# Optimization experiments

Hardware: AMD Instinct MI355X
Metric: run time of the kernel (lower is better)

The kernel has to match this reference:

```python
import jax, jax.numpy as jnp
import numpy as np

N = 50000   # nodes
E = 800000  # directed edges
IN, H1, H2, OUT = 128, 64, 32, 40
K = 2       # SGConv hops


def setup_inputs() -> dict:
    key = jax.random.key(0)
    ks = jax.random.split(key, 8)
    x = jax.random.normal(ks[0], (N, IN), dtype=jnp.float32)
    edge_index = jax.random.randint(ks[1], (2, E), 0, N, dtype=jnp.int64)
    s = lambda k, shp, fan: jax.random.normal(k, shp, dtype=jnp.float32) / np.sqrt(fan)
    return {
        "x": x,
        "edge_index": edge_index,
        "W1": s(ks[2], (IN, H1), IN), "b1": jnp.zeros((H1,), jnp.float32),
        "W2": s(ks[3], (H1, H2), H1), "b2": jnp.zeros((H2,), jnp.float32),
        "Wf": s(ks[4], (H2, OUT), H2), "bf": jnp.zeros((OUT,), jnp.float32),
    }


def _gcn_norm(edge_index, num_nodes):
    # add self-loops, then norm = d^{-1/2}[src] * d^{-1/2}[dst], d over targets
    loop = jnp.arange(num_nodes, dtype=edge_index.dtype)
    src = jnp.concatenate([edge_index[0], loop])
    dst = jnp.concatenate([edge_index[1], loop])
    deg = jax.ops.segment_sum(jnp.ones_like(src, dtype=jnp.float32), dst,
                              num_segments=num_nodes)
    dinv = jnp.where(deg > 0, jax.lax.rsqrt(deg), 0.0)
    norm = dinv[src] * dinv[dst]  # [E + N]
    return src, dst, norm


def _propagate_k(x, src, dst, norm, num_nodes, k):
    for _ in range(k):
        x = jax.ops.segment_sum(x[src] * norm[:, None], dst,
                                num_segments=num_nodes)
    return x


def reference(x, edge_index, W1, b1, W2, b2, Wf, bf):
    num_nodes = x.shape[0]
    src, dst, norm = _gcn_norm(edge_index, num_nodes)
    # SGConv layer 1: A_hat^K x, then linear, then relu
    h = _propagate_k(x, src, dst, norm, num_nodes, K)
    h = jax.nn.relu(h @ W1 + b1)
    # SGConv layer 2
    h = _propagate_k(h, src, dst, norm, num_nodes, K)
    h = jax.nn.relu(h @ W2 + b2)
    embedding = h
    logits = h @ Wf + bf
    return (embedding, logits)
```

## Files before the change

### kernel.cpp

```cpp
#include <hip/hip_runtime.h>

#define NN 50000
#define NE 800000
#define IN_F 128
#define H1_F 64
#define H2_F 32
#define OUT_F 40

#define BSH 7
#define NBKT 391
#define CAPA 4032
#define CHUNK 4096
#define NCH ((NE + CHUNK - 1) / CHUNK)

static inline int cdiv(int a, int b) { return (a + b - 1) / b; }

__global__ void initcur_k(int* __restrict__ gCursor) {
    int b = blockIdx.x * 256 + threadIdx.x;
    if (b < NBKT) gCursor[b] = b * CAPA;
}

__global__ __launch_bounds__(256)
void binA_k(const int* __restrict__ src, const int* __restrict__ dst,
            uint2* __restrict__ pairs, int* __restrict__ gCursor) {
    __shared__ int hist[512], incl[512], runSt[512], lcur[512], baseSh[512];
    __shared__ uint2 stage[CHUNK];
    const int t = threadIdx.x;
    const int e0 = blockIdx.x * CHUNK;
    const int n = min(CHUNK, NE - e0);

    hist[t] = 0; hist[t + 256] = 0;
    __syncthreads();
    for (int i = t; i < n; i += 256) {
        int d = dst[e0 + i];
        atomicAdd(&hist[d >> BSH], 1);
    }
    __syncthreads();
    incl[t] = hist[t]; incl[t + 256] = hist[t + 256];
    __syncthreads();
    for (int off = 1; off < 512; off <<= 1) {
        int v0 = (t >= off) ? incl[t - off] : 0;
        int v1 = (t + 256 >= off) ? incl[t + 256 - off] : 0;
        __syncthreads();
        incl[t] += v0; incl[t + 256] += v1;
        __syncthreads();
    }
    runSt[t] = incl[t] - hist[t];   runSt[t + 256] = incl[t + 256] - hist[t + 256];
    lcur[t]  = runSt[t];            lcur[t + 256]  = runSt[t + 256];
    __syncthreads();
    for (int i = t; i < n; i += 256) {
        int s = src[e0 + i], d = dst[e0 + i];
        int b = d >> BSH;
        int p = atomicAdd(&lcur[b], 1);
        stage[p] = make_uint2((unsigned)s, (unsigned)d);
    }
    for (int b = t; b < NBKT; b += 256) {
        int c = hist[b];
        baseSh[b] = c ? atomicAdd(&gCursor[b], c) : 0;
    }
    __syncthreads();
    for (int i = t; i < n; i += 256) {
        uint2 p = stage[i];
        int b = (int)(p.y >> BSH);
        int gp = baseSh[b] + (i - runSt[b]);
        if (gp < (b + 1) * CAPA) pairs[gp] = p;
    }
}

__global__ __launch_bounds__(512)
void segscan_k(const int* __restrict__ gCursor, int* __restrict__ segBase) {
    __shared__ int sh[512], orig[512];
    int t = threadIdx.x;
    int c = 0;
    if (t < NBKT) {
        c = gCursor[t] - t * CAPA;
        c = max(0, min(c, CAPA));
    }
    sh[t] = c; orig[t] = c;
    __syncthreads();
    for (int off = 1; off < 512; off <<= 1) {
        int v = (t >= off) ? sh[t - off] : 0;
        __syncthreads();
        sh[t] += v;
        __syncthreads();
    }
    if (t < NBKT) segBase[t] = sh[t] - orig[t];
}

__global__ __launch_bounds__(256)
void binB_k(const uint2* __restrict__ pairs, const int* __restrict__ gCursor,
            const int* __restrict__ segBase, int* __restrict__ cursor,
            float* __restrict__ dinv, int* __restrict__ csr) {
    const int b = blockIdx.x;
    const int nodeBase = b << BSH;
    const int nNodes = min(128, NN - nodeBase);
    int count = gCursor[b] - b * CAPA;
    count = max(0, min(count, CAPA));
    const int seg = segBase[b];
    __shared__ int hist[128], incl[128], lcur[128];
    const int t = threadIdx.x;
    if (t < 128) hist[t] = 0;
    __syncthreads();
    const uint2* bp = pairs + (size_t)b * CAPA;
    for (int i = t; i < count; i += 256) {
        int d = (int)bp[i].y - nodeBase;
        atomicAdd(&hist[d], 1);
    }
    __syncthreads();
    if (t < 128) incl[t] = hist[t];
    __syncthreads();
    for (int off = 1; off < 128; off <<= 1) {
        int v = (t < 128 && t >= off) ? incl[t - off] : 0;
        __syncthreads();
        if (t < 128) incl[t] += v;
        __syncthreads();
    }
    if (t < nNodes) {
        cursor[nodeBase + t] = seg + incl[t];
        dinv[nodeBase + t]   = rsqrtf((float)hist[t] + 1.0f);
        lcur[t] = seg + incl[t] - hist[t];
    }
    __syncthreads();
    for (int i = t; i < count; i += 256) {
        uint2 p = bp[i];
        int d = (int)p.y - nodeBase;
        int pos = atomicAdd(&lcur[d], 1);
        csr[pos] = (int)p.x;
    }
}

template<int K, int F, int CT, int RPT, int BLOCK, bool BIAS, bool SCALE>
__global__ __launch_bounds__(BLOCK)
void gemm_tile_k(const float* __restrict__ X, const float* __restrict__ W,
                 const float* __restrict__ b, const float* __restrict__ dinv,
                 float* __restrict__ Y) {
    constexpr int RT = BLOCK / CT;
    constexpr int TR = RT * RPT;
    constexpr int KT = 32;
    constexpr int KPAD = KT + 1;
    __shared__ float Xs[TR][KPAD];
    __shared__ float Wsh[KT][F];
    const int rowBase = blockIdx.x * TR;
    const int tc = threadIdx.x % CT;
    const int tr = threadIdx.x / CT;

    float acc[RPT][4];
    #pragma unroll
    for (int i = 0; i < RPT; ++i)
        #pragma unroll
        for (int j = 0; j < 4; ++j) acc[i][j] = 0.0f;

    for (int k0 = 0; k0 < K; k0 += KT) {
        constexpr int XL4 = TR * KT / 4;
        for (int l = threadIdx.x; l < XL4; l += BLOCK) {
            int r  = l / (KT / 4);
            int kk = (l % (KT / 4)) * 4;
            float4 v = make_float4(0.f, 0.f, 0.f, 0.f);
            int gr = rowBase + r;
            if (gr < NN) v = *reinterpret_cast<const float4*>(X + (size_t)gr * K + k0 + kk);
            Xs[r][kk + 0] = v.x; Xs[r][kk + 1] = v.y;
            Xs[r][kk + 2] = v.z; Xs[r][kk + 3] = v.w;
        }
        constexpr int WL4 = KT * F / 4;
        for (int l = threadIdx.x; l < WL4; l += BLOCK) {
            int kk = l / (F / 4);
            int c  = (l % (F / 4)) * 4;
            *reinterpret_cast<float4*>(&Wsh[kk][c]) =
                *reinterpret_cast<const float4*>(W + (size_t)(k0 + kk) * F + c);
        }
        __syncthreads();
        #pragma unroll
        for (int kk = 0; kk < KT; ++kk) {
            float wv[4];
            *reinterpret_cast<float4*>(wv) = *reinterpret_cast<const float4*>(&Wsh[kk][tc * 4]);
            #pragma unroll
            for (int i = 0; i < RPT; ++i) {
                float a = Xs[tr * RPT + i][kk];
                acc[i][0] = fmaf(a, wv[0], acc[i][0]);
                acc[i][1] = fmaf(a, wv[1], acc[i][1]);
                acc[i][2] = fmaf(a, wv[2], acc[i][2]);
                acc[i][3] = fmaf(a, wv[3], acc[i][3]);
            }
        }
        __syncthreads();
    }
    #pragma unroll
    for (int i = 0; i < RPT; ++i) {
        int gr = rowBase + tr * RPT + i;
        if (gr < NN) {
            float sc = SCALE ? dinv[gr] : 1.0f;
            float4 v;
            v.x = acc[i][0]; v.y = acc[i][1]; v.z = acc[i][2]; v.w = acc[i][3];
            if (BIAS) {
                v.x += b[tc * 4 + 0]; v.y += b[tc * 4 + 1];
                v.z += b[tc * 4 + 2]; v.w += b[tc * 4 + 3];
            }
            v.x *= sc; v.y *= sc; v.z *= sc; v.w *= sc;
            *reinterpret_cast<float4*>(Y + (size_t)gr * F + tc * 4) = v;
        }
    }
}

template<int F, bool SQ, bool EPI>
__global__ __launch_bounds__(256)
void pull4_k(const float* __restrict__ in, const int* __restrict__ csr,
             const int* __restrict__ cursor, const float* __restrict__ dinv,
             const float* __restrict__ b, float* __restrict__ out) {
    constexpr int LPN = F / 4;
    constexpr int NPB = 256 / LPN;
    const int t = threadIdx.x;
    const int node = blockIdx.x * NPB + t / LPN;
    const int col  = (t % LPN) * 4;
    if (node >= NN) return;
    const int beg = (node == 0) ? 0 : cursor[node - 1];
    const int end = cursor[node];
    const float* base = in + (size_t)node * F + col;
    float4 a0 = *reinterpret_cast<const float4*>(base);
    float4 a1 = make_float4(0.f, 0.f, 0.f, 0.f);
    int k = beg;
    for (; k + 1 < end; k += 2) {
        int s0 = csr[k], s1 = csr[k + 1];
        float4 v0 = *reinterpret_cast<const float4*>(in + (size_t)s0 * F + col);
        float4 v1 = *reinterpret_cast<const float4*>(in + (size_t)s1 * F + col);
        a0.x += v0.x; a0.y += v0.y; a0.z += v0.z; a0.w += v0.w;
        a1.x += v1.x; a1.y += v1.y; a1.z += v1.z; a1.w += v1.w;
    }
    if (k < end) {
        int s0 = csr[k];
        float4 v0 = *reinterpret_cast<const float4*>(in + (size_t)s0 * F + col);
        a0.x += v0.x; a0.y += v0.y; a0.z += v0.z; a0.w += v0.w;
    }
    float sc = dinv[node];
    if (SQ) sc *= sc;
    float4 r;
    r.x = (a0.x + a1.x) * sc; r.y = (a0.y + a1.y) * sc;
    r.z = (a0.z + a1.z) * sc; r.w = (a0.w + a1.w) * sc;
    if (EPI) {
        const float4 bv = *reinterpret_cast<const float4*>(b + col);
        r.x = fmaxf(r.x + bv.x, 0.f); r.y = fmaxf(r.y + bv.y, 0.f);
        r.z = fmaxf(r.z + bv.z, 0.f); r.w = fmaxf(r.w + bv.w, 0.f);
    }
    *reinterpret_cast<float4*>(out + (size_t)node * F + col) = r;
}

extern "C" void kernel_launch(void* const* d_in, const int* in_sizes, int n_in,
                              void* d_out, int out_size, void* d_ws, size_t ws_size,
                              hipStream_t stream) {
    const float* x  = (const float*)d_in[0];
    const int*   ei = (const int*)d_in[1];
    const float* W1 = (const float*)d_in[2];
    const float* b1 = (const float*)d_in[3];
    const float* W2 = (const float*)d_in[4];
    const float* b2 = (const float*)d_in[5];
    const float* Wf = (const float*)d_in[6];
    const float* bf = (const float*)d_in[7];

    float* out    = (float*)d_out;
    float* embOut = out;
    float* logits = out + (size_t)NN * H2_F;

    const int* src = ei;
    const int* dst = ei + NE;

    float* ws       = (float*)d_ws;
    float* dinv     = ws;
    int*   cursor   = (int*)(ws + NN);
    int*   csr      = cursor + NN;
    int*   gCursor  = csr + NE;
    int*   segBase  = gCursor + 512;
    float* bufA     = (float*)(segBase + 512);
    float* bufB     = bufA + (size_t)NN * 64;
    uint2* pairs    = (uint2*)bufB;

    initcur_k<<<cdiv(NBKT, 256), 256, 0, stream>>>(gCursor);
    binA_k<<<NCH, 256, 0, stream>>>(src, dst, pairs, gCursor);
    segscan_k<<<1, 512, 0, stream>>>(gCursor, segBase);
    binB_k<<<NBKT, 256, 0, stream>>>(pairs, gCursor, segBase, cursor, dinv, csr);

    gemm_tile_k<IN_F, H1_F, 16, 4, 256, false, true>
        <<<cdiv(NN, 64), 256, 0, stream>>>(x, W1, nullptr, dinv, bufA);
    pull4_k<H1_F, true, false>
        <<<cdiv(NN, 256 / (H1_F / 4)), 256, 0, stream>>>(bufA, csr, cursor, dinv, nullptr, bufB);
    pull4_k<H1_F, false, true>
        <<<cdiv(NN, 256 / (H1_F / 4)), 256, 0, stream>>>(bufB, csr, cursor, dinv, b1, bufA);

    gemm_tile_k<H1_F, H2_F, 8, 2, 256, false, true>
        <<<cdiv(NN, 64), 256, 0, stream>>>(bufA, W2, nullptr, dinv, bufB);
    pull4_k<H2_F, true, false>
        <<<cdiv(NN, 256 / (H2_F / 4)), 256, 0, stream>>>(bufB, csr, cursor, dinv, nullptr, bufA);
    pull4_k<H2_F, false, true>
        <<<cdiv(NN, 256 / (H2_F / 4)), 256, 0, stream>>>(bufA, csr, cursor, dinv, b2, embOut);

    gemm_tile_k<H2_F, OUT_F, 10, 2, 320, true, false>
        <<<cdiv(NN, 64), 320, 0, stream>>>(embOut, Wf, bf, nullptr, logits);
}
```

Before: 245.1 us.

## Fuse second-hop aggregation with the following dense GEMM and widen gather unroll

The second propagation hop of each layer now runs in one kernel together with the next linear layer. Each block aggregates 64 nodes into shared memory and multiplies them by W2 (or Wf) held in shared memory. This removes two standalone GEMM launches and the global round trip of the intermediate activations. The neighbour gather loop also moves from two to four independent accumulators to expose more memory-level parallelism. The cost is more registers and shared memory per block, and all 256 threads of a block wait at a barrier before the GEMM phase.

```diff
diff --git a/kernel.cpp b/kernel.cpp
--- a/kernel.cpp
+++ b/kernel.cpp
@@ -201,11 +201,11 @@
     }
 }
 
-template<int F, bool SQ, bool EPI>
+template<int F>
 __global__ __launch_bounds__(256)
 void pull4_k(const float* __restrict__ in, const int* __restrict__ csr,
              const int* __restrict__ cursor, const float* __restrict__ dinv,
-             const float* __restrict__ b, float* __restrict__ out) {
+             float* __restrict__ out) {
     constexpr int LPN = F / 4;
     constexpr int NPB = 256 / LPN;
     const int t = threadIdx.x;
@@ -214,33 +214,197 @@
     if (node >= NN) return;
     const int beg = (node == 0) ? 0 : cursor[node - 1];
     const int end = cursor[node];
-    const float* base = in + (size_t)node * F + col;
-    float4 a0 = *reinterpret_cast<const float4*>(base);
+    float4 a0 = *reinterpret_cast<const float4*>(in + (size_t)node * F + col);
     float4 a1 = make_float4(0.f, 0.f, 0.f, 0.f);
+    float4 a2 = make_float4(0.f, 0.f, 0.f, 0.f);
+    float4 a3 = make_float4(0.f, 0.f, 0.f, 0.f);
     int k = beg;
-    for (; k + 1 < end; k += 2) {
-        int s0 = csr[k], s1 = csr[k + 1];
+    for (; k + 3 < end; k += 4) {
+        int s0 = csr[k], s1 = csr[k + 1], s2 = csr[k + 2], s3 = csr[k + 3];
         float4 v0 = *reinterpret_cast<const float4*>(in + (size_t)s0 * F + col);
         float4 v1 = *reinterpret_cast<const float4*>(in + (size_t)s1 * F + col);
+        float4 v2 = *reinterpret_cast<const float4*>(in + (size_t)s2 * F + col);
+        float4 v3 = *reinterpret_cast<const float4*>(in + (size_t)s3 * F + col);
         a0.x += v0.x; a0.y += v0.y; a0.z += v0.z; a0.w += v0.w;
         a1.x += v1.x; a1.y += v1.y; a1.z += v1.z; a1.w += v1.w;
-    }
-    if (k < end) {
+        a2.x += v2.x; a2.y += v2.y; a2.z += v2.z; a2.w += v2.w;
+        a3.x += v3.x; a3.y += v3.y; a3.z += v3.z; a3.w += v3.w;
+    }
+    for (; k < end; ++k) {
         int s0 = csr[k];
         float4 v0 = *reinterpret_cast<const float4*>(in + (size_t)s0 * F + col);
         a0.x += v0.x; a0.y += v0.y; a0.z += v0.z; a0.w += v0.w;
     }
-    float sc = dinv[node];
-    if (SQ) sc *= sc;
+    float sc = dinv[node]; sc *= sc;
     float4 r;
-    r.x = (a0.x + a1.x) * sc; r.y = (a0.y + a1.y) * sc;
-    r.z = (a0.z + a1.z) * sc; r.w = (a0.w + a1.w) * sc;
-    if (EPI) {
-        const float4 bv = *reinterpret_cast<const float4*>(b + col);
-        r.x = fmaxf(r.x + bv.x, 0.f); r.y = fmaxf(r.y + bv.y, 0.f);
-        r.z = fmaxf(r.z + bv.z, 0.f); r.w = fmaxf(r.w + bv.w, 0.f);
-    }
+    r.x = (a0.x + a1.x + a2.x + a3.x) * sc;
+    r.y = (a0.y + a1.y + a2.y + a3.y) * sc;
+    r.z = (a0.z + a1.z + a2.z + a3.z) * sc;
+    r.w = (a0.w + a1.w + a2.w + a3.w) * sc;
     *reinterpret_cast<float4*>(out + (size_t)node * F + col) = r;
+}
+
+__global__ __launch_bounds__(256)
+void pullgemm2_k(const float* __restrict__ in, const int* __restrict__ csr,
+                 const int* __restrict__ cursor, const float* __restrict__ dinv,
+                 const float* __restrict__ b1, const float* __restrict__ W2,
+                 float* __restrict__ outT) {
+    __shared__ float hs[64][68];
+    __shared__ float W2s[64][32];
+    const int t = threadIdx.x;
+    for (int i = t; i < 64 * 32 / 4; i += 256)
+        reinterpret_cast<float4*>(&W2s[0][0])[i] = reinterpret_cast<const float4*>(W2)[i];
+    const int nodeBase = blockIdx.x * 64;
+    #pragma unroll
+    for (int pass = 0; pass < 4; ++pass) {
+        const int nb = pass * 16 + t / 16;
+        const int node = nodeBase + nb;
+        const int col = (t % 16) * 4;
+        float4 r = make_float4(0.f, 0.f, 0.f, 0.f);
+        if (node < NN) {
+            const int beg = (node == 0) ? 0 : cursor[node - 1];
+            const int end = cursor[node];
+            float4 a0 = *reinterpret_cast<const float4*>(in + (size_t)node * 64 + col);
+            float4 a1 = make_float4(0.f, 0.f, 0.f, 0.f);
+            float4 a2 = make_float4(0.f, 0.f, 0.f, 0.f);
+            float4 a3 = make_float4(0.f, 0.f, 0.f, 0.f);
+            int k = beg;
+            for (; k + 3 < end; k += 4) {
+                int s0 = csr[k], s1 = csr[k + 1], s2 = csr[k + 2], s3 = csr[k + 3];
+                float4 v0 = *reinterpret_cast<const float4*>(in + (size_t)s0 * 64 + col);
+                float4 v1 = *reinterpret_cast<const float4*>(in + (size_t)s1 * 64 + col);
+                float4 v2 = *reinterpret_cast<const float4*>(in + (size_t)s2 * 64 + col);
+                float4 v3 = *reinterpret_cast<const float4*>(in + (size_t)s3 * 64 + col);
+                a0.x += v0.x; a0.y += v0.y; a0.z += v0.z; a0.w += v0.w;
+                a1.x += v1.x; a1.y += v1.y; a1.z += v1.z; a1.w += v1.w;
+                a2.x += v2.x; a2.y += v2.y; a2.z += v2.z; a2.w += v2.w;
+                a3.x += v3.x; a3.y += v3.y; a3.z += v3.z; a3.w += v3.w;
+            }
+            for (; k < end; ++k) {
+                int s0 = csr[k];
+                float4 v0 = *reinterpret_cast<const float4*>(in + (size_t)s0 * 64 + col);
+                a0.x += v0.x; a0.y += v0.y; a0.z += v0.z; a0.w += v0.w;
+            }
+            const float sc = dinv[node];
+            const float4 bv = *reinterpret_cast<const float4*>(b1 + col);
+            r.x = fmaxf((a0.x + a1.x + a2.x + a3.x) * sc + bv.x, 0.f);
+            r.y = fmaxf((a0.y + a1.y + a2.y + a3.y) * sc + bv.y, 0.f);
+            r.z = fmaxf((a0.z + a1.z + a2.z + a3.z) * sc + bv.z, 0.f);
+            r.w = fmaxf((a0.w + a1.w + a2.w + a3.w) * sc + bv.w, 0.f);
+        }
+        *reinterpret_cast<float4*>(&hs[nb][col]) = r;
+    }
+    __syncthreads();
+    const int r = t / 4;
+    const int c0 = (t % 4) * 8;
+    float acc[8];
+    #pragma unroll
+    for (int j = 0; j < 8; ++j) acc[j] = 0.f;
+    #pragma unroll 4
+    for (int k = 0; k < 64; k += 4) {
+        float4 av = *reinterpret_cast<const float4*>(&hs[r][k]);
+        #pragma unroll
+        for (int kk = 0; kk < 4; ++kk) {
+            float a = (&av.x)[kk];
+            float4 w0 = *reinterpret_cast<const float4*>(&W2s[k + kk][c0]);
+            float4 w1 = *reinterpret_cast<const float4*>(&W2s[k + kk][c0 + 4]);
+            acc[0] = fmaf(a, w0.x, acc[0]); acc[1] = fmaf(a, w0.y, acc[1]);
+            acc[2] = fmaf(a, w0.z, acc[2]); acc[3] = fmaf(a, w0.w, acc[3]);
+            acc[4] = fmaf(a, w1.x, acc[4]); acc[5] = fmaf(a, w1.y, acc[5]);
+            acc[6] = fmaf(a, w1.z, acc[6]); acc[7] = fmaf(a, w1.w, acc[7]);
+        }
+    }
+    const int node = nodeBase + r;
+    if (node < NN) {
+        const float sc = dinv[node];
+        float4 o0, o1;
+        o0.x = acc[0] * sc; o0.y = acc[1] * sc; o0.z = acc[2] * sc; o0.w = acc[3] * sc;
+        o1.x = acc[4] * sc; o1.y = acc[5] * sc; o1.z = acc[6] * sc; o1.w = acc[7] * sc;
+        *reinterpret_cast<float4*>(outT + (size_t)node * 32 + c0)     = o0;
+        *reinterpret_cast<float4*>(outT + (size_t)node * 32 + c0 + 4) = o1;
+    }
+}
+
+__global__ __launch_bounds__(256)
+void pullgemmF_k(const float* __restrict__ in, const int* __restrict__ csr,
+                 const int* __restrict__ cursor, const float* __restrict__ dinv,
+                 const float* __restrict__ b2, const float* __restrict__ Wf,
+                 const float* __restrict__ bf, float* __restrict__ embOut,
+                 float* __restrict__ logits) {
+    __shared__ float es[64][36];
+    __shared__ float Wfs[32][40];
+    __shared__ float bfs[40];
+    const int t = threadIdx.x;
+    for (int i = t; i < 32 * 40 / 4; i += 256)
+        reinterpret_cast<float4*>(&Wfs[0][0])[i] = reinterpret_cast<const float4*>(Wf)[i];
+    if (t < 40) bfs[t] = bf[t];
+    const int nodeBase = blockIdx.x * 64;
+    #pragma unroll
+    for (int pass = 0; pass < 2; ++pass) {
+        const int nb = pass * 32 + t / 8;
+        const int node = nodeBase + nb;
+        const int col = (t % 8) * 4;
+        float4 r = make_float4(0.f, 0.f, 0.f, 0.f);
+        if (node < NN) {
+            const int beg = (node == 0) ? 0 : cursor[node - 1];
+            const int end = cursor[node];
+            float4 a0 = *reinterpret_cast<const float4*>(in + (size_t)node * 32 + col);
+            float4 a1 = make_float4(0.f, 0.f, 0.f, 0.f);
+            float4 a2 = make_float4(0.f, 0.f, 0.f, 0.f);
+            float4 a3 = make_float4(0.f, 0.f, 0.f, 0.f);
+            int k = beg;
+            for (; k + 3 < end; k += 4) {
+                int s0 = csr[k], s1 = csr[k + 1], s2 = csr[k + 2], s3 = csr[k + 3];
+                float4 v0 = *reinterpret_cast<const float4*>(in + (size_t)s0 * 32 + col);
+                float4 v1 = *reinterpret_cast<const float4*>(in + (size_t)s1 * 32 + col);
+                float4 v2 = *reinterpret_cast<const float4*>(in + (size_t)s2 * 32 + col);
+                float4 v3 = *reinterpret_cast<const float4*>(in + (size_t)s3 * 32 + col);
+                a0.x += v0.x; a0.y += v0.y; a0.z += v0.z; a0.w += v0.w;
+                a1.x += v1.x; a1.y += v1.y; a1.z += v1.z; a1.w += v1.w;
+                a2.x += v2.x; a2.y += v2.y; a2.z += v2.z; a2.w += v2.w;
+                a3.x += v3.x; a3.y += v3.y; a3.z += v3.z; a3.w += v3.w;
+            }
+            for (; k < end; ++k) {
+                int s0 = csr[k];
+                float4 v0 = *reinterpret_cast<const float4*>(in + (size_t)s0 * 32 + col);
+                a0.x += v0.x; a0.y += v0.y; a0.z += v0.z; a0.w += v0.w;
+            }
+            const float sc = dinv[node];
+            const float4 bv = *reinterpret_cast<const float4*>(b2 + col);
+            r.x = fmaxf((a0.x + a1.x + a2.x + a3.x) * sc + bv.x, 0.f);
+            r.y = fmaxf((a0.y + a1.y + a2.y + a3.y) * sc + bv.y, 0.f);
+            r.z = fmaxf((a0.z + a1.z + a2.z + a3.z) * sc + bv.z, 0.f);
+            r.w = fmaxf((a0.w + a1.w + a2.w + a3.w) * sc + bv.w, 0.f);
+            *reinterpret_cast<float4*>(embOut + (size_t)node * 32 + col) = r;
+        }
+        *reinterpret_cast<float4*>(&es[nb][col]) = r;
+    }
+    __syncthreads();
+    const int r = t / 4;
+    const int c0 = (t % 4) * 10;
+    float acc[10];
+    #pragma unroll
+    for (int j = 0; j < 10; ++j) acc[j] = bfs[c0 + j];
+    #pragma unroll 4
+    for (int k = 0; k < 32; k += 4) {
+        float4 av = *reinterpret_cast<const float4*>(&es[r][k]);
+        #pragma unroll
+        for (int kk = 0; kk < 4; ++kk) {
+            float a = (&av.x)[kk];
+            #pragma unroll
+            for (int j = 0; j < 10; ++j)
+                acc[j] = fmaf(a, Wfs[k + kk][c0 + j], acc[j]);
+        }
+    }
+    const int node = nodeBase + r;
+    if (node < NN) {
+        float* lp = logits + (size_t)node * 40 + c0;
+        #pragma unroll
+        for (int j = 0; j < 10; j += 2) {
+            float2 o; o.x = acc[j]; o.y = acc[j + 1];
+            *reinterpret_cast<float2*>(lp + j) = o;
+        }
+    }
 }
 
 extern "C" void kernel_launch(void* const* d_in, const int* in_sizes, int n_in,
@@ -279,18 +443,13 @@
 
     gemm_tile_k<IN_F, H1_F, 16, 4, 256, false, true>
         <<<cdiv(NN, 64), 256, 0, stream>>>(x, W1, nullptr, dinv, bufA);
-    pull4_k<H1_F, true, false>
-        <<<cdiv(NN, 256 / (H1_F / 4)), 256, 0, stream>>>(bufA, csr, cursor, dinv, nullptr, bufB);
-    pull4_k<H1_F, false, true>
-        <<<cdiv(NN, 256 / (H1_F / 4)), 256, 0, stream>>>(bufB, csr, cursor, dinv, b1, bufA);
-
-    gemm_tile_k<H1_F, H2_F, 8, 2, 256, false, true>
-        <<<cdiv(NN, 64), 256, 0, stream>>>(bufA, W2, nullptr, dinv, bufB);
-    pull4_k<H2_F, true, false>
-        <<<cdiv(NN, 256 / (H2_F / 4)), 256, 0, stream>>>(bufB, csr, cursor, dinv, nullptr, bufA);
-    pull4_k<H2_F, false, true>
-        <<<cdiv(NN, 256 / (H2_F / 4)), 256, 0, stream>>>(bufA, csr, cursor, dinv, b2, embOut);
-
-    gemm_tile_k<H2_F, OUT_F, 10, 2, 320, true, false>
-        <<<cdiv(NN, 64), 320, 0, stream>>>(embOut, Wf, bf, nullptr, logits);
-}
+    pull4_k<H1_F>
+        <<<cdiv(NN, 256 / (H1_F / 4)), 256, 0, stream>>>(bufA, csr, cursor, dinv, bufB);
+    pullgemm2_k
+        <<<cdiv(NN, 64), 256, 0, stream>>>(bufB, csr, cursor, dinv, b1, W2, bufA);
+
+    pull4_k<H2_F>
+        <<<cdiv(NN, 256 / (H2_F / 4)), 256, 0, stream>>>(bufA, csr, cursor, dinv, bufB);
+    pullgemmF_k
+        <<<cdiv(NN, 64), 256, 0, stream>>>(bufB, csr, cursor, dinv, b2, Wf, bf, embOut, logits);
+}
```

Result: no change. 240.4 us (-1.9%).
